# Performance work log

Measured on AMD Instinct MI355X. Metric: run time of the kernel, lower is better.

The kernel has to match this reference:

```python
import jax, jax.numpy as jnp
import numpy as np

N, D, E = 16384, 2048, 64          # tokens, d_model, n_experts
G = 8                               # n_expert_group
TOP_K = 8                           # experts selected per token
TOP_K_GROUP = 4                     # groups selected per token


def setup_inputs() -> dict:
    key = jax.random.key(0)
    k1, k2 = jax.random.split(key)
    x = jax.random.normal(k1, (N, D), dtype=jnp.float32)
    W = jax.random.normal(k2, (E, D), dtype=jnp.float32) * 0.02  # Linear weight
    b = jnp.zeros((E,), dtype=jnp.float32)                        # Linear bias
    bias = jnp.zeros((1, E), dtype=jnp.float32)                   # aux-loss-free routing bias
    return {"x": x, "W": W, "b": b, "bias": bias}


def reference(x, W, b, bias):
    n = x.shape[0]
    # linear + sigmoid
    score2weights = jax.nn.sigmoid(x @ W.T + b)       # [N, E]
    score = score2weights + bias                      # routing score with bias
    # group view
    score_g = score.reshape(n, G, -1)                 # [N, G, E/G]
    w_g = score2weights.reshape(n, G, -1)
    # group score = sum of top min(2, top_k) expert scores within each group
    top2, _ = jax.lax.top_k(score_g, min(2, TOP_K))   # [N, G, 2]
    group_score = top2.sum(axis=-1)                   # [N, G]
    # select top groups, build group mask (scatter)
    _, gidx = jax.lax.top_k(group_score, TOP_K_GROUP) # [N, TOP_K_GROUP]
    mask = jnp.zeros((n, G), score.dtype).at[jnp.arange(n)[:, None], gidx].set(1.0)
    # mask out non-selected groups, flatten back to expert dim
    score_m = (score_g * mask[..., None]).reshape(n, -1)   # [N, E]
    w_m = (w_g * mask[..., None]).reshape(n, -1)
    # final per-token expert selection + weight gather
    _, idx = jax.lax.top_k(score_m, TOP_K)            # [N, TOP_K] int32
    weights = jnp.take_along_axis(w_m, idx, axis=1)   # [N, TOP_K]
    return weights, idx
```

## Files before the change

kernel.cpp:

```cpp
#include <hip/hip_runtime.h>
#include <math.h>

#define DIM   2048
#define NEXP  64
#define NGRP  8
#define GSIZE 8
#define TOPK  8
#define TOPKG 4

#define TPB1  1024
#define NKS   8
#define KSL   (DIM / NKS)
#define SMSTR 1092

#define TAU_E 6e-5f
#define TAU_G 1.2e-4f
#define NEG_INF (-3.4e38f)
#define WLOFF 16
#define WT_OFF (1 << 18)

typedef __attribute__((ext_vector_type(8)))  short bf16x8;
typedef __attribute__((ext_vector_type(16))) float f32x16;

union FragU { bf16x8 v; unsigned short u[8]; };

static __device__ __forceinline__ unsigned short bf16_rne(float f) {
    unsigned u = __builtin_bit_cast(unsigned, f);
    u += 0x7FFFu + ((u >> 16) & 1u);
    return (unsigned short)(u >> 16);
}
static __device__ __forceinline__ float bf16_to_f(unsigned short h) {
    unsigned u = ((unsigned)h) << 16;
    return __builtin_bit_cast(float, u);
}

__global__ __launch_bounds__(256) void prep_kernel(
    const float* __restrict__ W, unsigned short* __restrict__ Wf,
    int* __restrict__ wl)
{
    const int g = blockIdx.x * 256 + threadIdx.x;
    const int e = g >> 11, k = g & 2047;
    const float w = W[g];
    const unsigned short hi = bf16_rne(w);
    const unsigned short lo = bf16_rne(w - bf16_to_f(hi));
    const int n2 = e >> 5, lcol = e & 31;
    const int kc = k >> 4, khalf = (k >> 3) & 1, j = k & 7;
    const int lane = (khalf << 5) | lcol;
    Wf[((((0 * 2 + n2) * 128 + kc) << 6) + lane) * 8 + j] = hi;
    Wf[((((1 * 2 + n2) * 128 + kc) << 6) + lane) * 8 + j] = lo;
    if (g < WLOFF) wl[g] = 0;
}

__global__ __launch_bounds__(TPB1, 4) void gate_kernel(
    const float* __restrict__ x,
    const unsigned short* __restrict__ Wf,
    const float* __restrict__ b,
    const float* __restrict__ bias,
    float* __restrict__ out_w,
    float* __restrict__ out_i,
    int* __restrict__ wl)
{
    __shared__ float sM[NKS * SMSTR];
    __shared__ float sS[64][65];

    const int tid  = threadIdx.x;
    const int w    = tid >> 6;
    const int lane = tid & 63;
    const int m    = w >> 3;
    const int ks   = w & 7;
    const int tok0 = blockIdx.x * 64;
    const int l31  = lane & 31, lh = lane >> 5;

    const float* xr = x + (size_t)(tok0 + 32 * m + l31) * DIM + ks * KSL + lh * 8;
    const bf16x8* Wfv = (const bf16x8*)Wf;

    f32x16 acc0, acc1;
#pragma unroll
    for (int z = 0; z < 16; ++z) { acc0[z] = 0.f; acc1[z] = 0.f; }

    float4 p0 = *(const float4*)(xr + 0);
    float4 p1 = *(const float4*)(xr + 4);
    float4 p2 = *(const float4*)(xr + 16);
    float4 p3 = *(const float4*)(xr + 20);

#pragma unroll 1
    for (int i = 0; i < 8; ++i) {
        const float4 c00 = p0, c01 = p1, c10 = p2, c11 = p3;
        if (i + 1 < 8) {
            p0 = *(const float4*)(xr + 32 * (i + 1) + 0);
            p1 = *(const float4*)(xr + 32 * (i + 1) + 4);
            p2 = *(const float4*)(xr + 32 * (i + 1) + 16);
            p3 = *(const float4*)(xr + 32 * (i + 1) + 20);
        }
        const int kc0 = ks * 16 + 2 * i;

#pragma unroll
        for (int c = 0; c < 2; ++c) {
            const int kc = kc0 + c;
            const float4 qa = c ? c10 : c00;
            const float4 qb = c ? c11 : c01;
            const float xv[8] = {qa.x, qa.y, qa.z, qa.w, qb.x, qb.y, qb.z, qb.w};
            FragU ah, al;
#pragma unroll
            for (int j = 0; j < 8; ++j) {
                const unsigned short h = bf16_rne(xv[j]);
                ah.u[j] = (short)h;
                al.u[j] = (short)bf16_rne(xv[j] - bf16_to_f(h));
            }
            const bf16x8 bh0 = Wfv[((0 * 2 + 0) * 128 + kc) * 64 + lane];
            const bf16x8 bh1 = Wfv[((0 * 2 + 1) * 128 + kc) * 64 + lane];
            const bf16x8 bl0 = Wfv[((1 * 2 + 0) * 128 + kc) * 64 + lane];
            const bf16x8 bl1 = Wfv[((1 * 2 + 1) * 128 + kc) * 64 + lane];

            acc0 = __builtin_amdgcn_mfma_f32_32x32x16_bf16(ah.v, bh0, acc0, 0, 0, 0);
            acc0 = __builtin_amdgcn_mfma_f32_32x32x16_bf16(ah.v, bl0, acc0, 0, 0, 0);
            acc0 = __builtin_amdgcn_mfma_f32_32x32x16_bf16(al.v, bh0, acc0, 0, 0, 0);
            acc1 = __builtin_amdgcn_mfma_f32_32x32x16_bf16(ah.v, bh1, acc1, 0, 0, 0);
            acc1 = __builtin_amdgcn_mfma_f32_32x32x16_bf16(ah.v, bl1, acc1, 0, 0, 0);
            acc1 = __builtin_amdgcn_mfma_f32_32x32x16_bf16(al.v, bh1, acc1, 0, 0, 0);
        }
    }

#pragma unroll
    for (int r = 0; r < 4; ++r) {
#pragma unroll
        for (int jj = 0; jj < 4; ++jj) {
            const int t16 = 8 * m + jj + 4 * lh;
            sM[ks * SMSTR + t16 * 68 + l31]      = acc0[4 * r + jj];
            sM[ks * SMSTR + t16 * 68 + l31 + 32] = acc1[4 * r + jj];
        }
        __syncthreads();
        {
            const int t16 = tid >> 6;
            const int e   = tid & 63;
            float sum = 0.f;
#pragma unroll
            for (int s = 0; s < NKS; ++s)
                sum += sM[s * SMSTR + t16 * 68 + e];
            const float logit = sum + b[e];
            const float wv = 1.0f / (1.0f + expf(-logit));
            const int t_blk = 32 * (t16 >> 3) + 8 * r + (t16 & 7);
            sS[t_blk][e] = wv + bias[e];
        }
        __syncthreads();
    }

    if (tid < 64) {
        const int t = tid;

        float gs[NGRP];
#pragma unroll
        for (int g = 0; g < NGRP; ++g) {
            float m1 = NEG_INF, m2 = NEG_INF;
#pragma unroll
            for (int j = 0; j < GSIZE; ++j) {
                const float v = sS[t][g * GSIZE + j];
                if (v > m1) { m2 = m1; m1 = v; }
                else if (v > m2) { m2 = v; }
            }
            gs[g] = m1 + m2;
        }

        unsigned gmask = 0u;
        float g4val = NEG_INF;
        for (int rr = 0; rr < TOPKG; ++rr) {
            float best = NEG_INF; int bi = 0;
#pragma unroll
            for (int g = 0; g < NGRP; ++g) {
                const float v = ((gmask >> g) & 1u) ? NEG_INF : gs[g];
                if (v > best) { best = v; bi = g; }
            }
            gmask |= 1u << bi;
            g4val = best;
        }
        float m5 = NEG_INF;
#pragma unroll
        for (int g = 0; g < NGRP; ++g)
            if (!((gmask >> g) & 1u) && gs[g] > m5) m5 = gs[g];
        const float margin_g = g4val - m5;

        unsigned long long chosen = 0ull;
        const size_t obase = (size_t)(tok0 + t) * TOPK;
        float vals[TOPK + 1];
        for (int rr = 0; rr < TOPK + 1; ++rr) {
            float best = NEG_INF; int bi = 0;
            for (int e = 0; e < NEXP; ++e) {
                float v = ((gmask >> (e >> 3)) & 1u) ? sS[t][e] : 0.0f;
                if ((chosen >> e) & 1ull) v = NEG_INF;
                if (v > best) { best = v; bi = e; }
            }
            vals[rr] = best;
            if (rr < TOPK) {
                chosen |= 1ull << (unsigned)bi;
                out_w[obase + rr] = ((gmask >> (bi >> 3)) & 1u)
                                  ? (sS[t][bi] - bias[bi]) : 0.0f;
                out_i[obase + rr] = (float)bi;
            }
        }
        float margin_e = 1e30f;
#pragma unroll
        for (int rr = 0; rr < TOPK; ++rr) {
            const float d = vals[rr] - vals[rr + 1];
            if (d < margin_e) margin_e = d;
        }

        if (margin_g < TAU_G || margin_e < TAU_E) {
            const int slot = atomicAdd(wl, 1);
            wl[WLOFF + slot] = tok0 + t;
        }
    }
}

__global__ __launch_bounds__(256) void gate_fix_kernel(
    const float* __restrict__ x,
    const float* __restrict__ W,
    const float* __restrict__ b,
    const float* __restrict__ bias,
    float* __restrict__ out_w,
    float* __restrict__ out_i,
    const int* __restrict__ wl)
{
    const int count = wl[0];

    __shared__ __align__(16) float sX[DIM];
    __shared__ double sPart[NEXP][4];
    __shared__ float  sS2[NEXP], sW2[NEXP];

    const int tid = threadIdx.x;
    const int e   = tid >> 2;
    const int s   = tid & 3;

    for (int widx = blockIdx.x; widx < count; widx += (int)gridDim.x) {
        const int tok = wl[WLOFF + widx];

        const float4* xr = (const float4*)(x + (size_t)tok * DIM);
        ((float4*)sX)[tid]       = xr[tid];
        ((float4*)sX)[tid + 256] = xr[tid + 256];
        __syncthreads();

        const float4* Wr = (const float4*)(W + (size_t)e * DIM);
        double a0 = 0., a1 = 0., a2 = 0., a3 = 0.;
#pragma unroll 8
        for (int mm = 0; mm < DIM / 16; ++mm) {
            const int c = mm * 4 + s;
            const float4 wv = Wr[c];
            const float4 xv = ((const float4*)sX)[c];
            a0 = fma((double)xv.x, (double)wv.x, a0);
            a1 = fma((double)xv.y, (double)wv.y, a1);
            a2 = fma((double)xv.z, (double)wv.z, a2);
            a3 = fma((double)xv.w, (double)wv.w, a3);
        }
        sPart[e][s] = (a0 + a1) + (a2 + a3);
        __syncthreads();

        if (tid < NEXP) {
            const double logit = ((sPart[tid][0] + sPart[tid][1])
                                + (sPart[tid][2] + sPart[tid][3])) + (double)b[tid];
            const float wv = (float)(1.0 / (1.0 + exp(-logit)));
            sW2[tid] = wv;
            sS2[tid] = wv + bias[tid];
        }
        __syncthreads();

        if (tid == 0) {
            float gs[NGRP];
#pragma unroll
            for (int g = 0; g < NGRP; ++g) {
                float m1 = NEG_INF, m2 = NEG_INF;
#pragma unroll
                for (int j = 0; j < GSIZE; ++j) {
                    const float v = sS2[g * GSIZE + j];
                    if (v > m1) { m2 = m1; m1 = v; }
                    else if (v > m2) { m2 = v; }
                }
                gs[g] = m1 + m2;
            }
            unsigned gmask = 0u;
            for (int rr = 0; rr < TOPKG; ++rr) {
                float best = NEG_INF; int bi = 0;
#pragma unroll
                for (int g = 0; g < NGRP; ++g) {
                    const float v = ((gmask >> g) & 1u) ? NEG_INF : gs[g];
                    if (v > best) { best = v; bi = g; }
                }
                gmask |= 1u << bi;
            }
            unsigned long long chosen = 0ull;
            const size_t obase = (size_t)tok * TOPK;
            for (int rr = 0; rr < TOPK; ++rr) {
                float best = NEG_INF; int bi = 0;
                for (int e2 = 0; e2 < NEXP; ++e2) {
                    float v = ((gmask >> (e2 >> 3)) & 1u) ? sS2[e2] : 0.0f;
                    if ((chosen >> e2) & 1ull) v = NEG_INF;
                    if (v > best) { best = v; bi = e2; }
                }
                chosen |= 1ull << (unsigned)bi;
                out_w[obase + rr] = ((gmask >> (bi >> 3)) & 1u) ? sW2[bi] : 0.0f;
                out_i[obase + rr] = (float)bi;
            }
        }
        __syncthreads();
    }
}

extern "C" void kernel_launch(void* const* d_in, const int* in_sizes, int n_in,
                              void* d_out, int out_size, void* d_ws, size_t ws_size,
                              hipStream_t stream) {
    const float* x    = (const float*)d_in[0];
    const float* W    = (const float*)d_in[1];
    const float* b    = (const float*)d_in[2];
    const float* bias = (const float*)d_in[3];

    const int n = in_sizes[0] / DIM;
    float* out_w = (float*)d_out;
    float* out_i = out_w + (size_t)n * TOPK;
    int*   wl    = (int*)d_ws;
    unsigned short* Wf = (unsigned short*)((char*)d_ws + WT_OFF);

    prep_kernel<<<dim3((NEXP * DIM) / 256), dim3(256), 0, stream>>>(W, Wf, wl);
    gate_kernel<<<dim3(n / 64), dim3(TPB1), 0, stream>>>(
        x, Wf, b, bias, out_w, out_i, wl);
    gate_fix_kernel<<<dim3(1024), dim3(256), 0, stream>>>(
        x, W, b, bias, out_w, out_i, wl);
}
```

Before: 279.5 us.

## Stage W tiles into LDS via async global_load_lds and switch split to fp16

Replaces per-wave global loads of the pre-split weight fragments with a double-buffered LDS staging scheme using global_load_lds: only one wave row loads each k-chunk, and both waves in the block reuse it after a barrier. The x loads become a 3-deep register prefetch with explicit vmcnt waits and sched barriers, and the chunk order is rotated per block to spread memory traffic. The hi/lo split also changes from bf16 to fp16 with packed round-toward-zero conversion, which is cheaper to compute. This adds two block barriers per iteration and depends on fp16 range holding for x and W. The two-term fp16 split uses RTZ rounding, so it carries a precision risk for values near the top-k selection ties.

```diff
diff --git a/kernel.cpp b/kernel.cpp
--- a/kernel.cpp
+++ b/kernel.cpp
@@ -19,19 +19,17 @@
 #define WLOFF 16
 #define WT_OFF (1 << 18)
 
-typedef __attribute__((ext_vector_type(8)))  short bf16x8;
-typedef __attribute__((ext_vector_type(16))) float f32x16;
-
-union FragU { bf16x8 v; unsigned short u[8]; };
-
-static __device__ __forceinline__ unsigned short bf16_rne(float f) {
-    unsigned u = __builtin_bit_cast(unsigned, f);
-    u += 0x7FFFu + ((u >> 16) & 1u);
-    return (unsigned short)(u >> 16);
-}
-static __device__ __forceinline__ float bf16_to_f(unsigned short h) {
-    unsigned u = ((unsigned)h) << 16;
-    return __builtin_bit_cast(float, u);
+typedef __attribute__((ext_vector_type(8)))  _Float16 f16x8;
+typedef __attribute__((ext_vector_type(16))) float    f32x16;
+
+#define SB() __builtin_amdgcn_sched_barrier(0)
+#define WAITVM(n) asm volatile("s_waitcnt vmcnt(" #n ")" ::: "memory")
+
+static __device__ __forceinline__ void gload_lds16(const void* g, void* l) {
+    __builtin_amdgcn_global_load_lds(
+        (const __attribute__((address_space(1))) unsigned*)g,
+        (__attribute__((address_space(3))) unsigned*)l,
+        16, 0, 0);
 }
 
 __global__ __launch_bounds__(256) void prep_kernel(
@@ -41,13 +39,15 @@
     const int g = blockIdx.x * 256 + threadIdx.x;
     const int e = g >> 11, k = g & 2047;
     const float w = W[g];
-    const unsigned short hi = bf16_rne(w);
-    const unsigned short lo = bf16_rne(w - bf16_to_f(hi));
+    const _Float16 hi = (_Float16)w;
+    const _Float16 lo = (_Float16)(w - (float)hi);
     const int n2 = e >> 5, lcol = e & 31;
     const int kc = k >> 4, khalf = (k >> 3) & 1, j = k & 7;
     const int lane = (khalf << 5) | lcol;
-    Wf[((((0 * 2 + n2) * 128 + kc) << 6) + lane) * 8 + j] = hi;
-    Wf[((((1 * 2 + n2) * 128 + kc) << 6) + lane) * 8 + j] = lo;
+    Wf[((((0 * 2 + n2) * 128 + kc) << 6) + lane) * 8 + j] =
+        __builtin_bit_cast(unsigned short, hi);
+    Wf[((((1 * 2 + n2) * 128 + kc) << 6) + lane) * 8 + j] =
+        __builtin_bit_cast(unsigned short, lo);
     if (g < WLOFF) wl[g] = 0;
 }
 
@@ -60,8 +60,9 @@
     float* __restrict__ out_i,
     int* __restrict__ wl)
 {
-    __shared__ float sM[NKS * SMSTR];
-    __shared__ float sS[64][65];
+    __shared__ __align__(16) char sLDS[65536];
+    float* sM = (float*)sLDS;
+    float (*sS)[65] = (float (*)[65])(sLDS + 34944);
 
     const int tid  = threadIdx.x;
     const int w    = tid >> 6;
@@ -70,56 +71,84 @@
     const int ks   = w & 7;
     const int tok0 = blockIdx.x * 64;
     const int l31  = lane & 31, lh = lane >> 5;
+    const int roff = (blockIdx.x >> 3) & 15;
 
     const float* xr = x + (size_t)(tok0 + 32 * m + l31) * DIM + ks * KSL + lh * 8;
-    const bf16x8* Wfv = (const bf16x8*)Wf;
+    const char* Wfb = (const char*)Wf;
 
     f32x16 acc0, acc1;
 #pragma unroll
     for (int z = 0; z < 16; ++z) { acc0[z] = 0.f; acc1[z] = 0.f; }
 
-    float4 p0 = *(const float4*)(xr + 0);
-    float4 p1 = *(const float4*)(xr + 4);
-    float4 p2 = *(const float4*)(xr + 16);
-    float4 p3 = *(const float4*)(xr + 20);
-
-#pragma unroll 1
-    for (int i = 0; i < 8; ++i) {
-        const float4 c00 = p0, c01 = p1, c10 = p2, c11 = p3;
-        if (i + 1 < 8) {
-            p0 = *(const float4*)(xr + 32 * (i + 1) + 0);
-            p1 = *(const float4*)(xr + 32 * (i + 1) + 4);
-            p2 = *(const float4*)(xr + 32 * (i + 1) + 16);
-            p3 = *(const float4*)(xr + 32 * (i + 1) + 20);
-        }
-        const int kc0 = ks * 16 + 2 * i;
-
-#pragma unroll
-        for (int c = 0; c < 2; ++c) {
-            const int kc = kc0 + c;
-            const float4 qa = c ? c10 : c00;
-            const float4 qb = c ? c11 : c01;
-            const float xv[8] = {qa.x, qa.y, qa.z, qa.w, qb.x, qb.y, qb.z, qb.w};
-            FragU ah, al;
-#pragma unroll
-            for (int j = 0; j < 8; ++j) {
-                const unsigned short h = bf16_rne(xv[j]);
-                ah.u[j] = (short)h;
-                al.u[j] = (short)bf16_rne(xv[j] - bf16_to_f(h));
-            }
-            const bf16x8 bh0 = Wfv[((0 * 2 + 0) * 128 + kc) * 64 + lane];
-            const bf16x8 bh1 = Wfv[((0 * 2 + 1) * 128 + kc) * 64 + lane];
-            const bf16x8 bl0 = Wfv[((1 * 2 + 0) * 128 + kc) * 64 + lane];
-            const bf16x8 bl1 = Wfv[((1 * 2 + 1) * 128 + kc) * 64 + lane];
-
-            acc0 = __builtin_amdgcn_mfma_f32_32x32x16_bf16(ah.v, bh0, acc0, 0, 0, 0);
-            acc0 = __builtin_amdgcn_mfma_f32_32x32x16_bf16(ah.v, bl0, acc0, 0, 0, 0);
-            acc0 = __builtin_amdgcn_mfma_f32_32x32x16_bf16(al.v, bh0, acc0, 0, 0, 0);
-            acc1 = __builtin_amdgcn_mfma_f32_32x32x16_bf16(ah.v, bh1, acc1, 0, 0, 0);
-            acc1 = __builtin_amdgcn_mfma_f32_32x32x16_bf16(ah.v, bl1, acc1, 0, 0, 0);
-            acc1 = __builtin_amdgcn_mfma_f32_32x32x16_bf16(al.v, bh1, acc1, 0, 0, 0);
-        }
-    }
+#define STAGE_B(tt, cc) do {                                                  \
+        char* dst_ = sLDS + (((tt) & 1) ? 32768 : 0) + ks * 4096;             \
+        const int kc_ = ks * 16 + (cc);                                       \
+        gload_lds16(Wfb + (size_t)((0 * 128 + kc_) * 64 + lane) * 16, dst_);  \
+        gload_lds16(Wfb + (size_t)((1 * 128 + kc_) * 64 + lane) * 16, dst_ + 1024); \
+        gload_lds16(Wfb + (size_t)((2 * 128 + kc_) * 64 + lane) * 16, dst_ + 2048); \
+        gload_lds16(Wfb + (size_t)((3 * 128 + kc_) * 64 + lane) * 16, dst_ + 3072); \
+    } while (0)
+
+    float4 pA[3], pB[3];
+    {
+        const int cc0 = roff;
+        pA[0] = *(const float4*)(xr + cc0 * 16);
+        pB[0] = *(const float4*)(xr + cc0 * 16 + 4);
+        SB();
+        if (m == 0) STAGE_B(0, cc0);
+        SB();
+        const int cc1 = (1 + roff) & 15;
+        pA[1] = *(const float4*)(xr + cc1 * 16);
+        pB[1] = *(const float4*)(xr + cc1 * 16 + 4);
+        SB();
+    }
+
+#pragma unroll
+    for (int t = 0; t < 16; ++t) {
+        if (t + 1 < 16) {
+            const int cc1 = (t + 1 + roff) & 15;
+            if (m == 0) STAGE_B(t + 1, cc1);
+        }
+        SB();
+        if (t + 2 < 16) {
+            const int cc2 = (t + 2 + roff) & 15;
+            pA[(t + 2) % 3] = *(const float4*)(xr + cc2 * 16);
+            pB[(t + 2) % 3] = *(const float4*)(xr + cc2 * 16 + 4);
+        }
+        if (t <= 13)      WAITVM(8);
+        else if (t == 14) WAITVM(6);
+        else              WAITVM(0);
+        SB();
+        __builtin_amdgcn_s_barrier();
+        SB();
+
+        const char* src = sLDS + ((t & 1) ? 32768 : 0) + ks * 4096;
+        const f16x8 bh0 = *(const f16x8*)(src + 0 * 1024 + lane * 16);
+        const f16x8 bh1 = *(const f16x8*)(src + 1 * 1024 + lane * 16);
+        const f16x8 bl0 = *(const f16x8*)(src + 2 * 1024 + lane * 16);
+        const f16x8 bl1 = *(const f16x8*)(src + 3 * 1024 + lane * 16);
+        const float4 qa = pA[t % 3], qb = pB[t % 3];
+        const float xv[8] = {qa.x, qa.y, qa.z, qa.w, qb.x, qb.y, qb.z, qb.w};
+        f16x8 ah, al;
+#pragma unroll
+        for (int j = 0; j < 8; j += 2) {
+            const auto h2 = __builtin_amdgcn_cvt_pkrtz(xv[j], xv[j + 1]);
+            const auto l2 = __builtin_amdgcn_cvt_pkrtz(xv[j]     - (float)h2.x,
+                                                       xv[j + 1] - (float)h2.y);
+            ah[j] = h2.x; ah[j + 1] = h2.y;
+            al[j] = l2.x; al[j + 1] = l2.y;
+        }
+        acc0 = __builtin_amdgcn_mfma_f32_32x32x16_f16(ah, bh0, acc0, 0, 0, 0);
+        acc0 = __builtin_amdgcn_mfma_f32_32x32x16_f16(ah, bl0, acc0, 0, 0, 0);
+        acc0 = __builtin_amdgcn_mfma_f32_32x32x16_f16(al, bh0, acc0, 0, 0, 0);
+        acc1 = __builtin_amdgcn_mfma_f32_32x32x16_f16(ah, bh1, acc1, 0, 0, 0);
+        acc1 = __builtin_amdgcn_mfma_f32_32x32x16_f16(ah, bl1, acc1, 0, 0, 0);
+        acc1 = __builtin_amdgcn_mfma_f32_32x32x16_f16(al, bh1, acc1, 0, 0, 0);
+        SB();
+        __builtin_amdgcn_s_barrier();
+        SB();
+    }
+#undef STAGE_B
 
 #pragma unroll
     for (int r = 0; r < 4; ++r) {
```

New measurement: 274.3 us. No clear change (-1.9%).
